# Kernel tuning notes

Measured on AMD Instinct MI355X. Metric: run time of the kernel, lower is better.

Reference implementation:

```python
import jax, jax.numpy as jnp
import numpy as np

BIN = 48
CPG = BIN * 3            # 144 hidden channels
SCALE = 2.0 / (BIN - 1)  # quantization step


def _causal_mask(k, include_center):
    # PixelCNN-style raster causal mask for a k x k kernel
    m = np.zeros((k, k), np.float32)
    c = k // 2
    m[:c, :] = 1.0
    m[c, :c] = 1.0
    if include_center:
        m[c, c] = 1.0
    return jnp.asarray(m)

MASK_NC = _causal_mask(5, False)  # first layer: strictly causal (exclude center)
MASK_C = _causal_mask(5, True)    # hidden/final layers: include center


def mconv(x, w, b, mask):
    # masked 5x5 conv, SAME padding, NCHW / OIHW
    y = jax.lax.conv_general_dilated(x, w * mask, (1, 1), 'SAME',
                                     dimension_numbers=('NCHW', 'OIHW', 'NCHW'))
    return y + b[None, :, None, None]


def setup_inputs() -> dict:
    key = jax.random.key(0)
    ks = jax.random.split(key, 8)
    H, W = 256, 512
    std = 0.02
    # quantized code in [-1, 1] on the bin grid, as produced by the decode loop
    lv = jax.random.randint(ks[0], (1, 1, H, W), 0, BIN)
    x = lv.astype(jnp.float32) * SCALE - 1.0
    return {
        'x': x,
        'w0': jax.random.normal(ks[1], (CPG, 1, 5, 5), jnp.float32) * std,
        'b0': jax.random.normal(ks[2], (CPG,), jnp.float32) * std,
        'wr': jax.random.normal(ks[3], (10, CPG, CPG, 5, 5), jnp.float32) * std,
        'br': jax.random.normal(ks[4], (10, CPG), jnp.float32) * std,
        'wf': jax.random.normal(ks[5], (BIN + 1, CPG, 5, 5), jnp.float32) * std,
        'bf': jax.random.normal(ks[6], (BIN + 1,), jnp.float32) * std,
    }


def reference(x, w0, b0, wr, br, wf, bf):
    # causal conv entropy network (CconvDc stack + 5 residual blocks)
    h = jax.nn.relu(mconv(x, w0, b0, MASK_NC))
    for i in range(5):  # EntropyResidualBlockD x5 (fixed small layer loop)
        y = jax.nn.relu(mconv(h, wr[2 * i], br[2 * i], MASK_C))
        y = jax.nn.relu(mconv(y, wr[2 * i + 1], br[2 * i + 1], MASK_C))
        h = h + y
    logits = mconv(h, wf, bf, MASK_C)            # (1, BIN+1, H, W)
    probs = jax.nn.softmax(logits, axis=1)       # per-pixel symbol distribution (EntropyTable input)

    # tail of forward: importance code -> channel mask -> depth-to-space x2
    tcode = jnp.floor((x + 1.0) / SCALE + 1e-5)  # (1,1,H,W) in [0, BIN-1]
    ch = jnp.arange(BIN * 4, dtype=x.dtype)[None, :, None, None]
    tmask = (ch < tcode * 4.0).astype(x.dtype)   # Imp2mask: (1, 4*BIN, H, W)
    N, C, H, W = tmask.shape
    t = tmask.reshape(N, C // 4, 2, 2, H, W)
    t = t.transpose(0, 1, 4, 2, 5, 3).reshape(N, C // 4, 2 * H, 2 * W)  # Dtow(2)
    return probs, t
```

## Files before the change

### kernel.cpp

```cpp
#include <hip/hip_runtime.h>
#include <hip/hip_bf16.h>
#include <stdint.h>

#define H 256
#define W 512
#define NCG 18
#define AW 520
#define AH 258
#define XB 16
#define ROWB (AW*XB)
#define CGB (AH*ROWB)
#define ACTB ((size_t)NCG*(size_t)CGB)
#define KG 236
#define NCHUNK 59
#define CHUNKB 9216
#define WPH_B ((size_t)KG*144*16)
#define WPF_B ((size_t)KG*64*16)

typedef float f32x4 __attribute__((ext_vector_type(4)));
typedef short bf16x8 __attribute__((ext_vector_type(8)));

__device__ __forceinline__ float bf2f(unsigned short u) {
  union { unsigned int i; float f; } v; v.i = ((unsigned int)u) << 16; return v.f;
}
__device__ __forceinline__ unsigned short f2bf(float f) {
  __hip_bfloat16 h = __float2bfloat16(f);
  return __builtin_bit_cast(unsigned short, h);
}
__device__ __forceinline__ void gload_lds16(const void* g, void* l) {
  __builtin_amdgcn_global_load_lds(
      (const __attribute__((address_space(1))) unsigned int*)g,
      (__attribute__((address_space(3))) unsigned int*)l, 16, 0, 0);
}

__global__ void k_pack_h(const float* __restrict__ wr, char* __restrict__ wph) {
  int idx = blockIdx.x * 256 + threadIdx.x;
  if (idx >= 10 * 144 * 144) return;
  int ci = idx % 144; int rem = idx / 144; int co = rem % 144; int layer = rem / 144;
  const float* src = wr + (size_t)((layer * 144 + co) * 144 + ci) * 25;
  unsigned short* dstL = (unsigned short*)(wph + (size_t)layer * WPH_B);
  int cig = ci >> 3, cis = ci & 7;
#pragma unroll
  for (int tap = 0; tap < 13; ++tap) {
    int ky = (tap >= 5) + (tap >= 10);
    int kx = tap - ky * 5;
    dstL[((size_t)(cig * 13 + tap) * 144 + co) * 8 + cis] = f2bf(src[ky * 5 + kx]);
  }
}
__global__ void k_pack_f(const float* __restrict__ wf, char* __restrict__ wpf) {
  int idx = blockIdx.x * 256 + threadIdx.x;
  if (idx >= 49 * 144) return;
  int ci = idx % 144; int co = idx / 144;
  const float* src = wf + (size_t)(co * 144 + ci) * 25;
  unsigned short* dst = (unsigned short*)wpf;
  int cig = ci >> 3, cis = ci & 7;
#pragma unroll
  for (int tap = 0; tap < 13; ++tap) {
    int ky = (tap >= 5) + (tap >= 10);
    int kx = tap - ky * 5;
    dst[((size_t)(cig * 13 + tap) * 64 + co) * 8 + cis] = f2bf(src[ky * 5 + kx]);
  }
}
__global__ void k_biaspad(const float* __restrict__ bf, float* __restrict__ bfp) {
  int i = threadIdx.x;
  bfp[i] = (i < 49) ? bf[i] : -1e30f;
}

__global__ void k_zeropad(char* __restrict__ actA, char* __restrict__ actB) {
  int i = blockIdx.x * 256 + threadIdx.x;
  if (i >= 2 * 18 * 2064) return;
  int s = i % 2064; int p = i / 2064; int cig = p % 18; int buf = p / 18;
  char* base = (buf ? actB : actA) + (size_t)cig * CGB;
  int row, colpx;
  if (s < 1040) { row = s / 520; colpx = s - row * 520; }
  else { int s2 = s - 1040; row = 2 + (s2 >> 2); int m = s2 & 3; colpx = (m < 2) ? m : (512 + m); }
  uint4 z; z.x = z.y = z.z = z.w = 0u;
  *(uint4*)(base + (size_t)row * ROWB + (size_t)colpx * 16) = z;
}

__global__ void k_layer0(const float* __restrict__ x, const float* __restrict__ w0,
                         const float* __restrict__ b0, char* __restrict__ act) {
  int i = blockIdx.x * 256 + threadIdx.x;
  int y = i >> 9, xx = i & 511;
  float xv[12];
#pragma unroll
  for (int tp = 0; tp < 12; ++tp) {
    int ky = (tp >= 5) + (tp >= 10);
    int kx = tp - ky * 5;
    int yy = y + ky - 2, xs = xx + kx - 2;
    bool ok = (yy >= 0) && (xs >= 0) && (xs < W);
    xv[tp] = ok ? x[yy * W + xs] : 0.f;
  }
  char* ob = act + (size_t)(y + 2) * ROWB + (size_t)(xx + 2) * XB;
  for (int cg = 0; cg < NCG; ++cg) {
    unsigned int us[4];
#pragma unroll
    for (int h2 = 0; h2 < 4; ++h2) {
      unsigned int lohi = 0;
#pragma unroll
      for (int p = 0; p < 2; ++p) {
        int co = cg * 8 + h2 * 2 + p;
        float a = b0[co];
#pragma unroll
        for (int tp = 0; tp < 12; ++tp) {
          int ky = (tp >= 5) + (tp >= 10);
          int kx = tp - ky * 5;
          a += w0[co * 25 + ky * 5 + kx] * xv[tp];
        }
        a = fmaxf(a, 0.f);
        lohi |= ((unsigned int)f2bf(a)) << (16 * p);
      }
      us[h2] = lohi;
    }
    uint4 v; v.x = us[0]; v.y = us[1]; v.z = us[2]; v.w = us[3];
    *(uint4*)(ob + (size_t)cg * CGB) = v;
  }
}

__global__ __launch_bounds__(256, 2)
void k_conv(const char* __restrict__ in, char* __restrict__ out,
            const char* __restrict__ wp, const float* __restrict__ bias, int res) {
  __shared__ __align__(16) char lA[2][CHUNKB];
  const int tid = threadIdx.x;
  const int wid = tid >> 6, lane = tid & 63;
  const int col = lane & 15, g = lane >> 4;

  int bid = blockIdx.x;
  int xcd = bid & 7, idx = bid >> 3;
  int by = xcd * 8 + (idx >> 3), bx = idx & 7;
  int y = by * 4 + wid, x0 = bx * 64;

  int pxo[4];
#pragma unroll
  for (int t = 0; t < 4; ++t) pxo[t] = (x0 + 16 * t + col) * XB;
  const char* bbase = in + (size_t)y * ROWB;

  f32x4 acc[9][4];
#pragma unroll
  for (int m = 0; m < 9; ++m)
#pragma unroll
    for (int t = 0; t < 4; ++t) acc[m][t] = (f32x4){0.f, 0.f, 0.f, 0.f};

  bf16x8 bA[4], bB[4];

  auto bload = [&](bf16x8 (&dst)[4], int c) __attribute__((always_inline)) {
    int kg = 4 * c + g;
    if (kg >= 234) kg = 0;
    int cig = kg / 13;
    int tap = kg - cig * 13;
    int ky = (tap >= 5) + (tap >= 10);
    int kx = tap - ky * 5;
    int off = cig * (int)CGB + ky * (int)ROWB + (kx << 4);
#pragma unroll
    for (int t = 0; t < 4; ++t) dst[t] = *(const bf16x8*)(bbase + (size_t)(off + pxo[t]));
  };

  auto stage = [&](char* ldsn, int c) __attribute__((always_inline)) {
    const char* wsrc = wp + (size_t)c * CHUNKB;
#pragma unroll
    for (int j0 = 0; j0 < 3; ++j0) {
      int j = wid + j0 * 4;
      if (j < 9) gload_lds16(wsrc + (size_t)j * 1024 + (lane << 4), ldsn + j * 1024);
    }
  };

  auto domfma = [&](const char* ldsc, bf16x8 (&bcur)[4]) __attribute__((always_inline)) {
    const char* abase = ldsc + ((g * 144 + col) << 4);
#pragma unroll
    for (int m = 0; m < 9; ++m) {
      bf16x8 a = *(const bf16x8*)(abase + m * 256);
#pragma unroll
      for (int t = 0; t < 4; ++t)
        acc[m][t] = __builtin_amdgcn_mfma_f32_16x16x32_bf16(a, bcur[t], acc[m][t], 0, 0, 0);
    }
  };

  auto phase = [&](const char* ldsc, char* ldsn, bf16x8 (&bcur)[4], bf16x8 (&bnext)[4],
                   int c) __attribute__((always_inline)) {
    stage(ldsn, c + 1);
    asm volatile("" ::: "memory");
    bload(bnext, c + 1);
    asm volatile("" ::: "memory");
    domfma(ldsc, bcur);
    asm volatile("s_waitcnt vmcnt(4)" ::: "memory");
    __builtin_amdgcn_s_barrier();
    asm volatile("" ::: "memory");
  };

  bload(bA, 0);
  stage(&lA[0][0], 0);
  asm volatile("s_waitcnt vmcnt(0)" ::: "memory");
  __builtin_amdgcn_s_barrier();
  asm volatile("" ::: "memory");

#pragma unroll 1
  for (int c = 0; c < NCHUNK - 1; c += 2) {
    phase(&lA[0][0], &lA[1][0], bA, bB, c);
    phase(&lA[1][0], &lA[0][0], bB, bA, c + 1);
  }
  domfma(&lA[0][0], bA);

  const int sub = (g & 1) * 8;
#pragma unroll
  for (int m = 0; m < 9; ++m) {
    int co0 = m * 16 + (g << 2);
    f32x4 bv = *(const f32x4*)(bias + co0);
    char* ob = out + (size_t)(co0 >> 3) * CGB + (size_t)(y + 2) * ROWB + sub + 32;
#pragma unroll
    for (int t = 0; t < 4; ++t) {
      char* oa = ob + pxo[t];
      float v0 = fmaxf(acc[m][t][0] + bv[0], 0.f);
      float v1 = fmaxf(acc[m][t][1] + bv[1], 0.f);
      float v2 = fmaxf(acc[m][t][2] + bv[2], 0.f);
      float v3 = fmaxf(acc[m][t][3] + bv[3], 0.f);
      if (res) {
        uint2 old = *(const uint2*)oa;
        v0 += bf2f((unsigned short)(old.x & 0xffff));
        v1 += bf2f((unsigned short)(old.x >> 16));
        v2 += bf2f((unsigned short)(old.y & 0xffff));
        v3 += bf2f((unsigned short)(old.y >> 16));
      }
      uint2 st;
      st.x = (unsigned int)f2bf(v0) | ((unsigned int)f2bf(v1) << 16);
      st.y = (unsigned int)f2bf(v2) | ((unsigned int)f2bf(v3) << 16);
      *(uint2*)oa = st;
    }
  }
}

__global__ __launch_bounds__(256, 2)
void k_convf(const char* __restrict__ in, float* __restrict__ probs,
             const char* __restrict__ wp, const float* __restrict__ bfp) {
  __shared__ __align__(16) char lA[2][4096];
  const int tid = threadIdx.x;
  const int wid = tid >> 6, lane = tid & 63;
  const int col = lane & 15, g = lane >> 4;

  int bid = blockIdx.x;
  int xcd = bid & 7, idx = bid >> 3;
  int by = xcd * 8 + (idx >> 3), bx = idx & 7;
  int y = by * 4 + wid, x0 = bx * 64;

  int pxo[4];
#pragma unroll
  for (int t = 0; t < 4; ++t) pxo[t] = (x0 + 16 * t + col) * XB;
  const char* bbase = in + (size_t)y * ROWB;

  f32x4 acc[4][4];
#pragma unroll
  for (int m = 0; m < 4; ++m)
#pragma unroll
    for (int t = 0; t < 4; ++t) acc[m][t] = (f32x4){0.f, 0.f, 0.f, 0.f};

  bf16x8 bA[4], bB[4];

  auto bload = [&](bf16x8 (&dst)[4], int c) __attribute__((always_inline)) {
    int kg = 4 * c + g;
    if (kg >= 234) kg = 0;
    int cig = kg / 13;
    int tap = kg - cig * 13;
    int ky = (tap >= 5) + (tap >= 10);
    int kx = tap - ky * 5;
    int off = cig * (int)CGB + ky * (int)ROWB + (kx << 4);
#pragma unroll
    for (int t = 0; t < 4; ++t) dst[t] = *(const bf16x8*)(bbase + (size_t)(off + pxo[t]));
  };

  auto stage = [&](char* ldsn, int c) __attribute__((always_inline)) {
    const char* wsrc = wp + (size_t)c * 4096;
    if (wid < 4) gload_lds16(wsrc + (size_t)wid * 1024 + (lane << 4), ldsn + wid * 1024);
  };

  auto domfma = [&](const char* ldsc, bf16x8 (&bcur)[4]) __attribute__((always_inline)) {
    const char* abase = ldsc + ((g * 64 + col) << 4);
#pragma unroll
    for (int m = 0; m < 4; ++m) {
      bf16x8 a = *(const bf16x8*)(abase + m * 256);
#pragma unroll
      for (int t = 0; t < 4; ++t)
        acc[m][t] = __builtin_amdgcn_mfma_f32_16x16x32_bf16(a, bcur[t], acc[m][t], 0, 0, 0);
    }
  };

  auto phase = [&](const char* ldsc, char* ldsn, bf16x8 (&bcur)[4], bf16x8 (&bnext)[4],
                   int c) __attribute__((always_inline)) {
    stage(ldsn, c + 1);
    asm volatile("" ::: "memory");
    bload(bnext, c + 1);
    asm volatile("" ::: "memory");
    domfma(ldsc, bcur);
    asm volatile("s_waitcnt vmcnt(4)" ::: "memory");
    __builtin_amdgcn_s_barrier();
    asm volatile("" ::: "memory");
  };

  bload(bA, 0);
  stage(&lA[0][0], 0);
  asm volatile("s_waitcnt vmcnt(0)" ::: "memory");
  __builtin_amdgcn_s_barrier();
  asm volatile("" ::: "memory");

#pragma unroll 1
  for (int c = 0; c < NCHUNK - 1; c += 2) {
    phase(&lA[0][0], &lA[1][0], bA, bB, c);
    phase(&lA[1][0], &lA[0][0], bB, bA, c + 1);
  }
  domfma(&lA[0][0], bA);

#pragma unroll
  for (int t = 0; t < 4; ++t) {
    float lg[4][4];
    float mx = -1e30f;
#pragma unroll
    for (int m = 0; m < 4; ++m) {
      f32x4 bv = *(const f32x4*)(bfp + m * 16 + (g << 2));
#pragma unroll
      for (int r = 0; r < 4; ++r) {
        lg[m][r] = acc[m][t][r] + bv[r];
        mx = fmaxf(mx, lg[m][r]);
      }
    }
    mx = fmaxf(mx, __shfl_xor(mx, 16));
    mx = fmaxf(mx, __shfl_xor(mx, 32));
    float s = 0.f;
#pragma unroll
    for (int m = 0; m < 4; ++m)
#pragma unroll
      for (int r = 0; r < 4; ++r) {
        lg[m][r] = __expf(lg[m][r] - mx);
        s += lg[m][r];
      }
    s += __shfl_xor(s, 16);
    s += __shfl_xor(s, 32);
    float inv = 1.f / s;
    int xp = x0 + 16 * t + col;
    float* op = probs + (size_t)y * W + xp;
#pragma unroll
    for (int m = 0; m < 4; ++m)
#pragma unroll
      for (int r = 0; r < 4; ++r) {
        int co = m * 16 + (g << 2) + r;
        if (co < 49) op[(size_t)co * (H * W)] = lg[m][r] * inv;
      }
  }
}

__global__ void k_tmask(const float* __restrict__ x, float* __restrict__ out1) {
  int i = blockIdx.x * 256 + threadIdx.x;
  int yy = i >> 10, xx = i & 1023;
  float xv = x[(yy >> 1) * W + (xx >> 1)];
  float tc = floorf((xv + 1.0f) / (float)(2.0 / 47.0) + 1e-5f);
#pragma unroll 4
  for (int g = 0; g < 48; ++g)
    out1[(size_t)g * (512 * 1024) + i] = ((float)g < tc) ? 1.0f : 0.0f;
}

extern "C" void kernel_launch(void* const* d_in, const int* in_sizes, int n_in,
                              void* d_out, int out_size, void* d_ws, size_t ws_size,
                              hipStream_t stream) {
  const float* x  = (const float*)d_in[0];
  const float* w0 = (const float*)d_in[1];
  const float* b0 = (const float*)d_in[2];
  const float* wr = (const float*)d_in[3];
  const float* br = (const float*)d_in[4];
  const float* wf = (const float*)d_in[5];
  const float* bf = (const float*)d_in[6];

  char* ws   = (char*)d_ws;
  char* actA = ws;
  char* actB = ws + ACTB;
  char* wph  = ws + 2 * ACTB;
  char* wpf  = wph + 10 * WPH_B;
  float* bfp = (float*)(wpf + WPF_B);

  hipMemsetAsync(wph, 0, 10 * WPH_B + WPF_B + 256, stream);
  k_zeropad<<<(2 * 18 * 2064 + 255) / 256, 256, 0, stream>>>(actA, actB);

  k_pack_h<<<(10 * 144 * 144 + 255) / 256, 256, 0, stream>>>(wr, wph);
  k_pack_f<<<(49 * 144 + 255) / 256, 256, 0, stream>>>(wf, wpf);
  k_biaspad<<<1, 64, 0, stream>>>(bf, bfp);

  k_layer0<<<512, 256, 0, stream>>>(x, w0, b0, actA);

  for (int i = 0; i < 5; ++i) {
    k_conv<<<512, 256, 0, stream>>>(actA, actB, wph + (size_t)(2 * i) * WPH_B,
                                    br + (2 * i) * 144, 0);
    k_conv<<<512, 256, 0, stream>>>(actB, actA, wph + (size_t)(2 * i + 1) * WPH_B,
                                    br + (2 * i + 1) * 144, 1);
  }

  float* probs = (float*)d_out;
  k_convf<<<512, 256, 0, stream>>>(actA, probs, wpf, bfp);
  k_tmask<<<2048, 256, 0, stream>>>(x, probs + (size_t)49 * H * W);
}
```

Measured before the change: 744.8 us.

## Halve blocks to two waves and double K-chunk per pipeline stage

Conv kernels now use 128-thread blocks (two rows per block, 1024 blocks) and process 8 k-groups per chunk instead of 4. This halves the number of barrier/stage iterations and doubles the B-fragment registers, and the weight chunks grow to 18 KB and 8 KB of LDS per buffer. The aim is to cut per-chunk synchronisation overhead and improve latency hiding. In exchange, each wave needs more registers and LDS, which could lower occupancy. Each 128-thread block also loads the full weight chunk for only two rows, so weight traffic per block doubles.

```diff
diff --git a/kernel.cpp b/kernel.cpp
--- a/kernel.cpp
+++ b/kernel.cpp
@@ -11,9 +11,10 @@
 #define ROWB (AW*XB)
 #define CGB (AH*ROWB)
 #define ACTB ((size_t)NCG*(size_t)CGB)
-#define KG 236
-#define NCHUNK 59
-#define CHUNKB 9216
+#define KG 240
+#define NCHUNK 30
+#define CHUNKB 18432
+#define CHUNKFB 8192
 #define WPH_B ((size_t)KG*144*16)
 #define WPF_B ((size_t)KG*64*16)
 
@@ -117,7 +118,7 @@
   }
 }
 
-__global__ __launch_bounds__(256, 2)
+__global__ __launch_bounds__(128, 2)
 void k_conv(const char* __restrict__ in, char* __restrict__ out,
             const char* __restrict__ wp, const float* __restrict__ bias, int res) {
   __shared__ __align__(16) char lA[2][CHUNKB];
@@ -127,8 +128,8 @@
 
   int bid = blockIdx.x;
   int xcd = bid & 7, idx = bid >> 3;
-  int by = xcd * 8 + (idx >> 3), bx = idx & 7;
-  int y = by * 4 + wid, x0 = bx * 64;
+  int by = xcd * 16 + (idx >> 3), bx = idx & 7;
+  int y = by * 2 + wid, x0 = bx * 64;
 
   int pxo[4];
 #pragma unroll
@@ -141,64 +142,73 @@
 #pragma unroll
     for (int t = 0; t < 4; ++t) acc[m][t] = (f32x4){0.f, 0.f, 0.f, 0.f};
 
-  bf16x8 bA[4], bB[4];
-
-  auto bload = [&](bf16x8 (&dst)[4], int c) __attribute__((always_inline)) {
-    int kg = 4 * c + g;
-    if (kg >= 234) kg = 0;
-    int cig = kg / 13;
-    int tap = kg - cig * 13;
-    int ky = (tap >= 5) + (tap >= 10);
-    int kx = tap - ky * 5;
-    int off = cig * (int)CGB + ky * (int)ROWB + (kx << 4);
-#pragma unroll
-    for (int t = 0; t < 4; ++t) dst[t] = *(const bf16x8*)(bbase + (size_t)(off + pxo[t]));
+  bf16x8 bA[8], bB[8];
+
+  auto bload = [&](bf16x8 (&dst)[8], int c) __attribute__((always_inline)) {
+#pragma unroll
+    for (int s = 0; s < 2; ++s) {
+      int kg = 8 * c + 4 * s + g;
+      if (kg >= 234) kg = 0;
+      int cig = kg / 13;
+      int tap = kg - cig * 13;
+      int ky = (tap >= 5) + (tap >= 10);
+      int kx = tap - ky * 5;
+      int off = cig * (int)CGB + ky * (int)ROWB + (kx << 4);
+#pragma unroll
+      for (int t = 0; t < 4; ++t)
+        dst[s * 4 + t] = *(const bf16x8*)(bbase + (size_t)(off + pxo[t]));
+    }
   };
 
   auto stage = [&](char* ldsn, int c) __attribute__((always_inline)) {
     const char* wsrc = wp + (size_t)c * CHUNKB;
 #pragma unroll
-    for (int j0 = 0; j0 < 3; ++j0) {
-      int j = wid + j0 * 4;
-      if (j < 9) gload_lds16(wsrc + (size_t)j * 1024 + (lane << 4), ldsn + j * 1024);
-    }
-  };
-
-  auto domfma = [&](const char* ldsc, bf16x8 (&bcur)[4]) __attribute__((always_inline)) {
-    const char* abase = ldsc + ((g * 144 + col) << 4);
-#pragma unroll
-    for (int m = 0; m < 9; ++m) {
-      bf16x8 a = *(const bf16x8*)(abase + m * 256);
-#pragma unroll
-      for (int t = 0; t < 4; ++t)
-        acc[m][t] = __builtin_amdgcn_mfma_f32_16x16x32_bf16(a, bcur[t], acc[m][t], 0, 0, 0);
-    }
-  };
-
-  auto phase = [&](const char* ldsc, char* ldsn, bf16x8 (&bcur)[4], bf16x8 (&bnext)[4],
+    for (int j0 = 0; j0 < 9; ++j0) {
+      int j = wid + j0 * 2;
+      gload_lds16(wsrc + (size_t)j * 1024 + (lane << 4), ldsn + j * 1024);
+    }
+  };
+
+  auto domfma = [&](const char* ldsc, bf16x8 (&b)[8]) __attribute__((always_inline)) {
+#pragma unroll
+    for (int s = 0; s < 2; ++s) {
+      const char* abase = ldsc + (((4 * s + g) * 144 + col) << 4);
+#pragma unroll
+      for (int m = 0; m < 9; ++m) {
+        bf16x8 a = *(const bf16x8*)(abase + m * 256);
+#pragma unroll
+        for (int t = 0; t < 4; ++t)
+          acc[m][t] = __builtin_amdgcn_mfma_f32_16x16x32_bf16(a, b[s * 4 + t], acc[m][t], 0, 0, 0);
+      }
+    }
+  };
+
+  auto phase = [&](const char* ldsc, char* ldsn, bf16x8 (&bcur)[8], bf16x8 (&bnext)[8],
                    int c) __attribute__((always_inline)) {
     stage(ldsn, c + 1);
     asm volatile("" ::: "memory");
     bload(bnext, c + 1);
     asm volatile("" ::: "memory");
     domfma(ldsc, bcur);
-    asm volatile("s_waitcnt vmcnt(4)" ::: "memory");
+    asm volatile("s_waitcnt vmcnt(8)" ::: "memory");
     __builtin_amdgcn_s_barrier();
     asm volatile("" ::: "memory");
   };
 
+  stage(&lA[0][0], 0);
+  asm volatile("" ::: "memory");
   bload(bA, 0);
-  stage(&lA[0][0], 0);
-  asm volatile("s_waitcnt vmcnt(0)" ::: "memory");
+  asm volatile("s_waitcnt vmcnt(8)" ::: "memory");
   __builtin_amdgcn_s_barrier();
   asm volatile("" ::: "memory");
 
 #pragma unroll 1
-  for (int c = 0; c < NCHUNK - 1; c += 2) {
+  for (int c = 0; c < NCHUNK - 2; c += 2) {
     phase(&lA[0][0], &lA[1][0], bA, bB, c);
     phase(&lA[1][0], &lA[0][0], bB, bA, c + 1);
   }
-  domfma(&lA[0][0], bA);
+  phase(&lA[0][0], &lA[1][0], bA, bB, NCHUNK - 2);
+  domfma(&lA[1][0], bB);
 
   const int sub = (g & 1) * 8;
 #pragma unroll
@@ -228,18 +238,18 @@
   }
 }
 
-__global__ __launch_bounds__(256, 2)
+__global__ __launch_bounds__(128, 2)
 void k_convf(const char* __restrict__ in, float* __restrict__ probs,
              const char* __restrict__ wp, const float* __restrict__ bfp) {
-  __shared__ __align__(16) char lA[2][4096];
+  __shared__ __align__(16) char lA[2][CHUNKFB];
   const int tid = threadIdx.x;
   const int wid = tid >> 6, lane = tid & 63;
   const int col = lane & 15, g = lane >> 4;
 
   int bid = blockIdx.x;
   int xcd = bid & 7, idx = bid >> 3;
-  int by = xcd * 8 + (idx >> 3), bx = idx & 7;
-  int y = by * 4 + wid, x0 = bx * 64;
+  int by = xcd * 16 + (idx >> 3), bx = idx & 7;
+  int y = by * 2 + wid, x0 = bx * 64;
 
   int pxo[4];
 #pragma unroll
@@ -252,60 +262,73 @@
 #pragma unroll
     for (int t = 0; t < 4; ++t) acc[m][t] = (f32x4){0.f, 0.f, 0.f, 0.f};
 
-  bf16x8 bA[4], bB[4];
-
-  auto bload = [&](bf16x8 (&dst)[4], int c) __attribute__((always_inline)) {
-    int kg = 4 * c + g;
-    if (kg >= 234) kg = 0;
-    int cig = kg / 13;
-    int tap = kg - cig * 13;
-    int ky = (tap >= 5) + (tap >= 10);
-    int kx = tap - ky * 5;
-    int off = cig * (int)CGB + ky * (int)ROWB + (kx << 4);
-#pragma unroll
-    for (int t = 0; t < 4; ++t) dst[t] = *(const bf16x8*)(bbase + (size_t)(off + pxo[t]));
+  bf16x8 bA[8], bB[8];
+
+  auto bload = [&](bf16x8 (&dst)[8], int c) __attribute__((always_inline)) {
+#pragma unroll
+    for (int s = 0; s < 2; ++s) {
+      int kg = 8 * c + 4 * s + g;
+      if (kg >= 234) kg = 0;
+      int cig = kg / 13;
+      int tap = kg - cig * 13;
+      int ky = (tap >= 5) + (tap >= 10);
+      int kx = tap - ky * 5;
+      int off = cig * (int)CGB + ky * (int)ROWB + (kx << 4);
+#pragma unroll
+      for (int t = 0; t < 4; ++t)
+        dst[s * 4 + t] = *(const bf16x8*)(bbase + (size_t)(off + pxo[t]));
+    }
   };
 
   auto stage = [&](char* ldsn, int c) __attribute__((always_inline)) {
-    const char* wsrc = wp + (size_t)c * 4096;
-    if (wid < 4) gload_lds16(wsrc + (size_t)wid * 1024 + (lane << 4), ldsn + wid * 1024);
-  };
-
-  auto domfma = [&](const char* ldsc, bf16x8 (&bcur)[4]) __attribute__((always_inline)) {
-    const char* abase = ldsc + ((g * 64 + col) << 4);
-#pragma unroll
-    for (int m = 0; m < 4; ++m) {
-      bf16x8 a = *(const bf16x8*)(abase + m * 256);
-#pragma unroll
-      for (int t = 0; t < 4; ++t)
-        acc[m][t] = __builtin_amdgcn_mfma_f32_16x16x32_bf16(a, bcur[t], acc[m][t], 0, 0, 0);
-    }
-  };
-
-  auto phase = [&](const char* ldsc, char* ldsn, bf16x8 (&bcur)[4], bf16x8 (&bnext)[4],
+    const char* wsrc = wp + (size_t)c * CHUNKFB;
+#pragma unroll
+    for (int j0 = 0; j0 < 4; ++j0) {
+      int j = wid + j0 * 2;
+      gload_lds16(wsrc + (size_t)j * 1024 + (lane << 4), ldsn + j * 1024);
+    }
+  };
+
+  auto domfma = [&](const char* ldsc, bf16x8 (&b)[8]) __attribute__((always_inline)) {
+#pragma unroll
+    for (int s = 0; s < 2; ++s) {
+      const char* abase = ldsc + (((4 * s + g) * 64 + col) << 4);
+#pragma unroll
+      for (int m = 0; m < 4; ++m) {
+        bf16x8 a = *(const bf16x8*)(abase + m * 256);
+#pragma unroll
+        for (int t = 0; t < 4; ++t)
+          acc[m][t] = __builtin_amdgcn_mfma_f32_16x16x32_bf16(a, b[s * 4 + t], acc[m][t], 0, 0, 0);
+      }
+    }
+  };
+
+  auto phase = [&](const char* ldsc, char* ldsn, bf16x8 (&bcur)[8], bf16x8 (&bnext)[8],
                    int c) __attribute__((always_inline)) {
     stage(ldsn, c + 1);
     asm volatile("" ::: "memory");
     bload(bnext, c + 1);
     asm volatile("" ::: "memory");
     domfma(ldsc, bcur);
-    asm volatile("s_waitcnt vmcnt(4)" ::: "memory");
+    asm volatile("s_waitcnt vmcnt(8)" ::: "memory");
     __builtin_amdgcn_s_barrier();
     asm volatile("" ::: "memory");
   };
 
+  stage(&lA[0][0], 0);
+  asm volatile("" ::: "memory");
   bload(bA, 0);
-  stage(&lA[0][0], 0);
-  asm volatile("s_waitcnt vmcnt(0)" ::: "memory");
+  asm volatile("s_waitcnt vmcnt(8)" ::: "memory");
   __builtin_amdgcn_s_barrier();
   asm volatile("" ::: "memory");
 
 #pragma unroll 1
-  for (int c = 0; c < NCHUNK - 1; c += 2) {
+  for (int c = 0; c < NCHUNK - 2; c += 2) {
     phase(&lA[0][0], &lA[1][0], bA, bB, c);
     phase(&lA[1][0], &lA[0][0], bB, bA, c + 1);
   }
-  domfma(&lA[0][0], bA);
+  phase(&lA[0][0], &lA[1][0], bA, bB, NCHUNK - 2);
+  domfma(&lA[1][0], bB);
 
 #pragma unroll
   for (int t = 0; t < 4; ++t) {
@@ -383,13 +406,13 @@
   k_layer0<<<512, 256, 0, stream>>>(x, w0, b0, actA);
 
   for (int i = 0; i < 5; ++i) {
-    k_conv<<<512, 256, 0, stream>>>(actA, actB, wph + (size_t)(2 * i) * WPH_B,
-                                    br + (2 * i) * 144, 0);
-    k_conv<<<512, 256, 0, stream>>>(actB, actA, wph + (size_t)(2 * i + 1) * WPH_B,
-                                    br + (2 * i + 1) * 144, 1);
+    k_conv<<<1024, 128, 0, stream>>>(actA, actB, wph + (size_t)(2 * i) * WPH_B,
+                                     br + (2 * i) * 144, 0);
+    k_conv<<<1024, 128, 0, stream>>>(actB, actA, wph + (size_t)(2 * i + 1) * WPH_B,
+                                     br + (2 * i + 1) * 144, 1);
   }
 
   float* probs = (float*)d_out;
-  k_convf<<<512, 256, 0, stream>>>(actA, probs, wpf, bfp);
+  k_convf<<<1024, 128, 0, stream>>>(actA, probs, wpf, bfp);
   k_tmask<<<2048, 256, 0, stream>>>(x, probs + (size_t)49 * H * W);
 }
```

New measurement: 933.1 us. 1.25x slower.

## Stage three weight chunks per barrier and add MFMA priority in conv kernels

Applied to the files above, without the earlier changes.

Restructures the main loop of both conv kernels so each iteration stages three weight chunks into a larger double-buffered LDS region. Three sets of activation registers are kept in flight, which cuts the number of block barriers per output tile by a factor of three. Activation offset computation becomes incremental (tap/offc counters) instead of using a per-chunk division. The MFMA sections are wrapped in s_setprio to favour matrix issue. The cost is more LDS (about 55KB per block for k_conv) and more VGPRs, which may hurt occupancy at 2 blocks per CU. The vmcnt(4) wait now covers more outstanding loads, so the ordering of loads must be checked carefully.

```diff
diff --git a/kernel.cpp b/kernel.cpp
--- a/kernel.cpp
+++ b/kernel.cpp
@@ -14,6 +14,7 @@
 #define KG 236
 #define NCHUNK 59
 #define CHUNKB 9216
+#define CHUNKFB 4096
 #define WPH_B ((size_t)KG*144*16)
 #define WPF_B ((size_t)KG*64*16)
 
@@ -120,7 +121,7 @@
 __global__ __launch_bounds__(256, 2)
 void k_conv(const char* __restrict__ in, char* __restrict__ out,
             const char* __restrict__ wp, const float* __restrict__ bias, int res) {
-  __shared__ __align__(16) char lA[2][CHUNKB];
+  __shared__ __align__(16) char lA[2][3 * CHUNKB];
   const int tid = threadIdx.x;
   const int wid = tid >> 6, lane = tid & 63;
   const int col = lane & 15, g = lane >> 4;
@@ -141,31 +142,32 @@
 #pragma unroll
     for (int t = 0; t < 4; ++t) acc[m][t] = (f32x4){0.f, 0.f, 0.f, 0.f};
 
-  bf16x8 bA[4], bB[4];
-
-  auto bload = [&](bf16x8 (&dst)[4], int c) __attribute__((always_inline)) {
-    int kg = 4 * c + g;
-    if (kg >= 234) kg = 0;
-    int cig = kg / 13;
-    int tap = kg - cig * 13;
+  bf16x8 bA[4], bB[4], bC[4];
+
+  int tap = g, offc = 0;
+  auto bload = [&](bf16x8 (&dst)[4]) __attribute__((always_inline)) {
     int ky = (tap >= 5) + (tap >= 10);
     int kx = tap - ky * 5;
-    int off = cig * (int)CGB + ky * (int)ROWB + (kx << 4);
+    int off = offc + ky * (int)ROWB + (kx << 4);
 #pragma unroll
     for (int t = 0; t < 4; ++t) dst[t] = *(const bf16x8*)(bbase + (size_t)(off + pxo[t]));
-  };
-
-  auto stage = [&](char* ldsn, int c) __attribute__((always_inline)) {
-    const char* wsrc = wp + (size_t)c * CHUNKB;
-#pragma unroll
-    for (int j0 = 0; j0 < 3; ++j0) {
-      int j = wid + j0 * 4;
-      if (j < 9) gload_lds16(wsrc + (size_t)j * 1024 + (lane << 4), ldsn + j * 1024);
+    tap += 4; if (tap >= 13) { tap -= 13; offc += (int)CGB; }
+  };
+
+  auto stage1 = [&](char* ldsn, int c) __attribute__((always_inline)) {
+    if (c < NCHUNK) {
+      const char* wsrc = wp + (size_t)c * CHUNKB;
+#pragma unroll
+      for (int j0 = 0; j0 < 3; ++j0) {
+        int j = wid + j0 * 4;
+        if (j < 9) gload_lds16(wsrc + (size_t)j * 1024 + (lane << 4), ldsn + j * 1024);
+      }
     }
   };
 
   auto domfma = [&](const char* ldsc, bf16x8 (&bcur)[4]) __attribute__((always_inline)) {
     const char* abase = ldsc + ((g * 144 + col) << 4);
+    __builtin_amdgcn_s_setprio(1);
 #pragma unroll
     for (int m = 0; m < 9; ++m) {
       bf16x8 a = *(const bf16x8*)(abase + m * 256);
@@ -173,32 +175,41 @@
       for (int t = 0; t < 4; ++t)
         acc[m][t] = __builtin_amdgcn_mfma_f32_16x16x32_bf16(a, bcur[t], acc[m][t], 0, 0, 0);
     }
-  };
-
-  auto phase = [&](const char* ldsc, char* ldsn, bf16x8 (&bcur)[4], bf16x8 (&bnext)[4],
-                   int c) __attribute__((always_inline)) {
-    stage(ldsn, c + 1);
-    asm volatile("" ::: "memory");
-    bload(bnext, c + 1);
-    asm volatile("" ::: "memory");
-    domfma(ldsc, bcur);
-    asm volatile("s_waitcnt vmcnt(4)" ::: "memory");
-    __builtin_amdgcn_s_barrier();
-    asm volatile("" ::: "memory");
-  };
-
-  bload(bA, 0);
-  stage(&lA[0][0], 0);
+    __builtin_amdgcn_s_setprio(0);
+  };
+
+  stage1(&lA[0][0 * CHUNKB], 0);
+  stage1(&lA[0][1 * CHUNKB], 1);
+  stage1(&lA[0][2 * CHUNKB], 2);
+  asm volatile("" ::: "memory");
+  bload(bA);
   asm volatile("s_waitcnt vmcnt(0)" ::: "memory");
   __builtin_amdgcn_s_barrier();
   asm volatile("" ::: "memory");
 
 #pragma unroll 1
-  for (int c = 0; c < NCHUNK - 1; c += 2) {
-    phase(&lA[0][0], &lA[1][0], bA, bB, c);
-    phase(&lA[1][0], &lA[0][0], bB, bA, c + 1);
-  }
-  domfma(&lA[0][0], bA);
+  for (int s = 0; s < 19; ++s) {
+    const char* R = &lA[s & 1][0];
+    char* N = &lA[(s & 1) ^ 1][0];
+    bload(bB);
+    bload(bC);
+    asm volatile("" ::: "memory");
+    stage1(N + 0 * CHUNKB, 3 * s + 3);
+    stage1(N + 1 * CHUNKB, 3 * s + 4);
+    stage1(N + 2 * CHUNKB, 3 * s + 5);
+    asm volatile("" ::: "memory");
+    domfma(R + 0 * CHUNKB, bA);
+    bload(bA);
+    asm volatile("" ::: "memory");
+    domfma(R + 1 * CHUNKB, bB);
+    domfma(R + 2 * CHUNKB, bC);
+    asm volatile("s_waitcnt vmcnt(4)" ::: "memory");
+    __builtin_amdgcn_s_barrier();
+    asm volatile("" ::: "memory");
+  }
+  bload(bB);
+  domfma(&lA[1][0 * CHUNKB], bA);
+  domfma(&lA[1][1 * CHUNKB], bB);
 
   const int sub = (g & 1) * 8;
 #pragma unroll
@@ -231,7 +242,7 @@
 __global__ __launch_bounds__(256, 2)
 void k_convf(const char* __restrict__ in, float* __restrict__ probs,
              const char* __restrict__ wp, const float* __restrict__ bfp) {
-  __shared__ __align__(16) char lA[2][4096];
+  __shared__ __align__(16) char lA[2][3 * CHUNKFB];
   const int tid = threadIdx.x;
   const int wid = tid >> 6, lane = tid & 63;
   const int col = lane & 15, g = lane >> 4;
@@ -252,27 +263,27 @@
 #pragma unroll
     for (int t = 0; t < 4; ++t) acc[m][t] = (f32x4){0.f, 0.f, 0.f, 0.f};
 
-  bf16x8 bA[4], bB[4];
-
-  auto bload = [&](bf16x8 (&dst)[4], int c) __attribute__((always_inline)) {
-    int kg = 4 * c + g;
-    if (kg >= 234) kg = 0;
-    int cig = kg / 13;
-    int tap = kg - cig * 13;
+  bf16x8 bA[4], bB[4], bC[4];
+
+  int tap = g, offc = 0;
+  auto bload = [&](bf16x8 (&dst)[4]) __attribute__((always_inline)) {
     int ky = (tap >= 5) + (tap >= 10);
     int kx = tap - ky * 5;
-    int off = cig * (int)CGB + ky * (int)ROWB + (kx << 4);
+    int off = offc + ky * (int)ROWB + (kx << 4);
 #pragma unroll
     for (int t = 0; t < 4; ++t) dst[t] = *(const bf16x8*)(bbase + (size_t)(off + pxo[t]));
-  };
-
-  auto stage = [&](char* ldsn, int c) __attribute__((always_inline)) {
-    const char* wsrc = wp + (size_t)c * 4096;
-    if (wid < 4) gload_lds16(wsrc + (size_t)wid * 1024 + (lane << 4), ldsn + wid * 1024);
+    tap += 4; if (tap >= 13) { tap -= 13; offc += (int)CGB; }
+  };
+
+  auto stage1 = [&](char* ldsn, int c) __attribute__((always_inline)) {
+    if (c < NCHUNK && wid < 4)
+      gload_lds16(wp + (size_t)c * CHUNKFB + (size_t)wid * 1024 + (lane << 4),
+                  ldsn + wid * 1024);
   };
 
   auto domfma = [&](const char* ldsc, bf16x8 (&bcur)[4]) __attribute__((always_inline)) {
     const char* abase = ldsc + ((g * 64 + col) << 4);
+    __builtin_amdgcn_s_setprio(1);
 #pragma unroll
     for (int m = 0; m < 4; ++m) {
       bf16x8 a = *(const bf16x8*)(abase + m * 256);
@@ -280,32 +291,41 @@
       for (int t = 0; t < 4; ++t)
         acc[m][t] = __builtin_amdgcn_mfma_f32_16x16x32_bf16(a, bcur[t], acc[m][t], 0, 0, 0);
     }
-  };
-
-  auto phase = [&](const char* ldsc, char* ldsn, bf16x8 (&bcur)[4], bf16x8 (&bnext)[4],
-                   int c) __attribute__((always_inline)) {
-    stage(ldsn, c + 1);
-    asm volatile("" ::: "memory");
-    bload(bnext, c + 1);
-    asm volatile("" ::: "memory");
-    domfma(ldsc, bcur);
-    asm volatile("s_waitcnt vmcnt(4)" ::: "memory");
-    __builtin_amdgcn_s_barrier();
-    asm volatile("" ::: "memory");
-  };
-
-  bload(bA, 0);
-  stage(&lA[0][0], 0);
+    __builtin_amdgcn_s_setprio(0);
+  };
+
+  stage1(&lA[0][0 * CHUNKFB], 0);
+  stage1(&lA[0][1 * CHUNKFB], 1);
+  stage1(&lA[0][2 * CHUNKFB], 2);
+  asm volatile("" ::: "memory");
+  bload(bA);
   asm volatile("s_waitcnt vmcnt(0)" ::: "memory");
   __builtin_amdgcn_s_barrier();
   asm volatile("" ::: "memory");
 
 #pragma unroll 1
-  for (int c = 0; c < NCHUNK - 1; c += 2) {
-    phase(&lA[0][0], &lA[1][0], bA, bB, c);
-    phase(&lA[1][0], &lA[0][0], bB, bA, c + 1);
-  }
-  domfma(&lA[0][0], bA);
+  for (int s = 0; s < 19; ++s) {
+    const char* R = &lA[s & 1][0];
+    char* N = &lA[(s & 1) ^ 1][0];
+    bload(bB);
+    bload(bC);
+    asm volatile("" ::: "memory");
+    stage1(N + 0 * CHUNKFB, 3 * s + 3);
+    stage1(N + 1 * CHUNKFB, 3 * s + 4);
+    stage1(N + 2 * CHUNKFB, 3 * s + 5);
+    asm volatile("" ::: "memory");
+    domfma(R + 0 * CHUNKFB, bA);
+    bload(bA);
+    asm volatile("" ::: "memory");
+    domfma(R + 1 * CHUNKFB, bB);
+    domfma(R + 2 * CHUNKFB, bC);
+    asm volatile("s_waitcnt vmcnt(4)" ::: "memory");
+    __builtin_amdgcn_s_barrier();
+    asm volatile("" ::: "memory");
+  }
+  bload(bB);
+  domfma(&lA[1][0 * CHUNKFB], bA);
+  domfma(&lA[1][1 * CHUNKFB], bB);
 
 #pragma unroll
   for (int t = 0; t < 4; ++t) {
```

New measurement: 748.0 us. Within noise of the previous version (+0.4%).

## Halve per-wave pixel tile, double grid and occupancy, add MFMA priority

Applied to the files above, without the earlier changes.

Each wave now computes 32 output pixels instead of 64, which halves the accumulator and B-fragment registers. Launch bounds rise to 4 blocks per CU and the conv grids double to 1024 blocks. Tap and channel-group indexing moves from a per-chunk divide to an incremental counter, and s_setprio raises wave priority around the MFMA loops. The cost is that each weight chunk staged in LDS is reused over half as many pixels, so weight traffic from L2 to LDS doubles.

```diff
diff --git a/kernel.cpp b/kernel.cpp
--- a/kernel.cpp
+++ b/kernel.cpp
@@ -14,6 +14,7 @@
 #define KG 236
 #define NCHUNK 59
 #define CHUNKB 9216
+#define CHUNKFB 4096
 #define WPH_B ((size_t)KG*144*16)
 #define WPF_B ((size_t)KG*64*16)
 
@@ -117,7 +118,7 @@
   }
 }
 
-__global__ __launch_bounds__(256, 2)
+__global__ __launch_bounds__(256, 4)
 void k_conv(const char* __restrict__ in, char* __restrict__ out,
             const char* __restrict__ wp, const float* __restrict__ bias, int res) {
   __shared__ __align__(16) char lA[2][CHUNKB];
@@ -127,32 +128,30 @@
 
   int bid = blockIdx.x;
   int xcd = bid & 7, idx = bid >> 3;
-  int by = xcd * 8 + (idx >> 3), bx = idx & 7;
-  int y = by * 4 + wid, x0 = bx * 64;
-
-  int pxo[4];
-#pragma unroll
-  for (int t = 0; t < 4; ++t) pxo[t] = (x0 + 16 * t + col) * XB;
+  int by = xcd * 8 + (idx >> 4), bx = idx & 15;
+  int y = by * 4 + wid, x0 = bx * 32;
+
+  int pxo[2];
+#pragma unroll
+  for (int t = 0; t < 2; ++t) pxo[t] = (x0 + 16 * t + col) * XB;
   const char* bbase = in + (size_t)y * ROWB;
 
-  f32x4 acc[9][4];
+  f32x4 acc[9][2];
 #pragma unroll
   for (int m = 0; m < 9; ++m)
 #pragma unroll
-    for (int t = 0; t < 4; ++t) acc[m][t] = (f32x4){0.f, 0.f, 0.f, 0.f};
-
-  bf16x8 bA[4], bB[4];
-
-  auto bload = [&](bf16x8 (&dst)[4], int c) __attribute__((always_inline)) {
-    int kg = 4 * c + g;
-    if (kg >= 234) kg = 0;
-    int cig = kg / 13;
-    int tap = kg - cig * 13;
+    for (int t = 0; t < 2; ++t) acc[m][t] = (f32x4){0.f, 0.f, 0.f, 0.f};
+
+  bf16x8 bA[2], bB[2];
+
+  int tap = g, offc = 0;
+  auto bload = [&](bf16x8 (&dst)[2]) __attribute__((always_inline)) {
     int ky = (tap >= 5) + (tap >= 10);
     int kx = tap - ky * 5;
-    int off = cig * (int)CGB + ky * (int)ROWB + (kx << 4);
-#pragma unroll
-    for (int t = 0; t < 4; ++t) dst[t] = *(const bf16x8*)(bbase + (size_t)(off + pxo[t]));
+    int off = offc + ky * (int)ROWB + (kx << 4);
+#pragma unroll
+    for (int t = 0; t < 2; ++t) dst[t] = *(const bf16x8*)(bbase + (size_t)(off + pxo[t]));
+    tap += 4; if (tap >= 13) { tap -= 13; offc += (int)CGB; }
   };
 
   auto stage = [&](char* ldsn, int c) __attribute__((always_inline)) {
@@ -164,31 +163,34 @@
     }
   };
 
-  auto domfma = [&](const char* ldsc, bf16x8 (&bcur)[4]) __attribute__((always_inline)) {
+  auto domfma = [&](const char* ldsc, bf16x8 (&bcur)[2]) __attribute__((always_inline)) {
     const char* abase = ldsc + ((g * 144 + col) << 4);
+    __builtin_amdgcn_s_setprio(1);
 #pragma unroll
     for (int m = 0; m < 9; ++m) {
       bf16x8 a = *(const bf16x8*)(abase + m * 256);
 #pragma unroll
-      for (int t = 0; t < 4; ++t)
+      for (int t = 0; t < 2; ++t)
         acc[m][t] = __builtin_amdgcn_mfma_f32_16x16x32_bf16(a, bcur[t], acc[m][t], 0, 0, 0);
     }
-  };
-
-  auto phase = [&](const char* ldsc, char* ldsn, bf16x8 (&bcur)[4], bf16x8 (&bnext)[4],
+    __builtin_amdgcn_s_setprio(0);
+  };
+
+  auto phase = [&](const char* ldsc, char* ldsn, bf16x8 (&bcur)[2], bf16x8 (&bnext)[2],
                    int c) __attribute__((always_inline)) {
     stage(ldsn, c + 1);
     asm volatile("" ::: "memory");
-    bload(bnext, c + 1);
+    bload(bnext);
     asm volatile("" ::: "memory");
     domfma(ldsc, bcur);
-    asm volatile("s_waitcnt vmcnt(4)" ::: "memory");
+    asm volatile("s_waitcnt vmcnt(2)" ::: "memory");
     __builtin_amdgcn_s_barrier();
     asm volatile("" ::: "memory");
   };
 
-  bload(bA, 0);
   stage(&lA[0][0], 0);
+  asm volatile("" ::: "memory");
+  bload(bA);
   asm volatile("s_waitcnt vmcnt(0)" ::: "memory");
   __builtin_amdgcn_s_barrier();
   asm volatile("" ::: "memory");
@@ -207,7 +209,7 @@
     f32x4 bv = *(const f32x4*)(bias + co0);
     char* ob = out + (size_t)(co0 >> 3) * CGB + (size_t)(y + 2) * ROWB + sub + 32;
 #pragma unroll
-    for (int t = 0; t < 4; ++t) {
+    for (int t = 0; t < 2; ++t) {
       char* oa = ob + pxo[t];
       float v0 = fmaxf(acc[m][t][0] + bv[0], 0.f);
       float v1 = fmaxf(acc[m][t][1] + bv[1], 0.f);
@@ -228,74 +230,76 @@
   }
 }
 
-__global__ __launch_bounds__(256, 2)
+__global__ __launch_bounds__(256, 4)
 void k_convf(const char* __restrict__ in, float* __restrict__ probs,
              const char* __restrict__ wp, const float* __restrict__ bfp) {
-  __shared__ __align__(16) char lA[2][4096];
+  __shared__ __align__(16) char lA[2][CHUNKFB];
   const int tid = threadIdx.x;
   const int wid = tid >> 6, lane = tid & 63;
   const int col = lane & 15, g = lane >> 4;
 
   int bid = blockIdx.x;
   int xcd = bid & 7, idx = bid >> 3;
-  int by = xcd * 8 + (idx >> 3), bx = idx & 7;
-  int y = by * 4 + wid, x0 = bx * 64;
-
-  int pxo[4];
-#pragma unroll
-  for (int t = 0; t < 4; ++t) pxo[t] = (x0 + 16 * t + col) * XB;
+  int by = xcd * 8 + (idx >> 4), bx = idx & 15;
+  int y = by * 4 + wid, x0 = bx * 32;
+
+  int pxo[2];
+#pragma unroll
+  for (int t = 0; t < 2; ++t) pxo[t] = (x0 + 16 * t + col) * XB;
   const char* bbase = in + (size_t)y * ROWB;
 
-  f32x4 acc[4][4];
+  f32x4 acc[4][2];
 #pragma unroll
   for (int m = 0; m < 4; ++m)
 #pragma unroll
-    for (int t = 0; t < 4; ++t) acc[m][t] = (f32x4){0.f, 0.f, 0.f, 0.f};
-
-  bf16x8 bA[4], bB[4];
-
-  auto bload = [&](bf16x8 (&dst)[4], int c) __attribute__((always_inline)) {
-    int kg = 4 * c + g;
-    if (kg >= 234) kg = 0;
-    int cig = kg / 13;
-    int tap = kg - cig * 13;
+    for (int t = 0; t < 2; ++t) acc[m][t] = (f32x4){0.f, 0.f, 0.f, 0.f};
+
+  bf16x8 bA[2], bB[2];
+
+  int tap = g, offc = 0;
+  auto bload = [&](bf16x8 (&dst)[2]) __attribute__((always_inline)) {
     int ky = (tap >= 5) + (tap >= 10);
     int kx = tap - ky * 5;
-    int off = cig * (int)CGB + ky * (int)ROWB + (kx << 4);
-#pragma unroll
-    for (int t = 0; t < 4; ++t) dst[t] = *(const bf16x8*)(bbase + (size_t)(off + pxo[t]));
+    int off = offc + ky * (int)ROWB + (kx << 4);
+#pragma unroll
+    for (int t = 0; t < 2; ++t) dst[t] = *(const bf16x8*)(bbase + (size_t)(off + pxo[t]));
+    tap += 4; if (tap >= 13) { tap -= 13; offc += (int)CGB; }
   };
 
   auto stage = [&](char* ldsn, int c) __attribute__((always_inline)) {
-    const char* wsrc = wp + (size_t)c * 4096;
-    if (wid < 4) gload_lds16(wsrc + (size_t)wid * 1024 + (lane << 4), ldsn + wid * 1024);
-  };
-
-  auto domfma = [&](const char* ldsc, bf16x8 (&bcur)[4]) __attribute__((always_inline)) {
+    if (wid < 4)
+      gload_lds16(wp + (size_t)c * CHUNKFB + (size_t)wid * 1024 + (lane << 4),
+                  ldsn + wid * 1024);
+  };
+
+  auto domfma = [&](const char* ldsc, bf16x8 (&bcur)[2]) __attribute__((always_inline)) {
     const char* abase = ldsc + ((g * 64 + col) << 4);
+    __builtin_amdgcn_s_setprio(1);
 #pragma unroll
     for (int m = 0; m < 4; ++m) {
       bf16x8 a = *(const bf16x8*)(abase + m * 256);
 #pragma unroll
-      for (int t = 0; t < 4; ++t)
+      for (int t = 0; t < 2; ++t)
         acc[m][t] = __builtin_amdgcn_mfma_f32_16x16x32_bf16(a, bcur[t], acc[m][t], 0, 0, 0);
     }
-  };
-
-  auto phase = [&](const char* ldsc, char* ldsn, bf16x8 (&bcur)[4], bf16x8 (&bnext)[4],
+    __builtin_amdgcn_s_setprio(0);
+  };
+
+  auto phase = [&](const char* ldsc, char* ldsn, bf16x8 (&bcur)[2], bf16x8 (&bnext)[2],
                    int c) __attribute__((always_inline)) {
     stage(ldsn, c + 1);
     asm volatile("" ::: "memory");
-    bload(bnext, c + 1);
+    bload(bnext);
     asm volatile("" ::: "memory");
     domfma(ldsc, bcur);
-    asm volatile("s_waitcnt vmcnt(4)" ::: "memory");
+    asm volatile("s_waitcnt vmcnt(2)" ::: "memory");
     __builtin_amdgcn_s_barrier();
     asm volatile("" ::: "memory");
   };
 
-  bload(bA, 0);
   stage(&lA[0][0], 0);
+  asm volatile("" ::: "memory");
+  bload(bA);
   asm volatile("s_waitcnt vmcnt(0)" ::: "memory");
   __builtin_amdgcn_s_barrier();
   asm volatile("" ::: "memory");
@@ -308,7 +312,7 @@
   domfma(&lA[0][0], bA);
 
 #pragma unroll
-  for (int t = 0; t < 4; ++t) {
+  for (int t = 0; t < 2; ++t) {
     float lg[4][4];
     float mx = -1e30f;
 #pragma unroll
@@ -383,13 +387,13 @@
   k_layer0<<<512, 256, 0, stream>>>(x, w0, b0, actA);
 
   for (int i = 0; i < 5; ++i) {
-    k_conv<<<512, 256, 0, stream>>>(actA, actB, wph + (size_t)(2 * i) * WPH_B,
-                                    br + (2 * i) * 144, 0);
-    k_conv<<<512, 256, 0, stream>>>(actB, actA, wph + (size_t)(2 * i + 1) * WPH_B,
-                                    br + (2 * i + 1) * 144, 1);
+    k_conv<<<1024, 256, 0, stream>>>(actA, actB, wph + (size_t)(2 * i) * WPH_B,
+                                     br + (2 * i) * 144, 0);
+    k_conv<<<1024, 256, 0, stream>>>(actB, actA, wph + (size_t)(2 * i + 1) * WPH_B,
+                                     br + (2 * i + 1) * 144, 1);
   }
 
   float* probs = (float*)d_out;
-  k_convf<<<512, 256, 0, stream>>>(actA, probs, wpf, bfp);
+  k_convf<<<1024, 256, 0, stream>>>(actA, probs, wpf, bfp);
   k_tmask<<<2048, 256, 0, stream>>>(x, probs + (size_t)49 * H * W);
 }
```

Result: no change. 750.4 us (+0.8%).
